# Optimization experiments

Hardware: AMD Instinct MI355X
Metric: run time of the kernel (lower is better)

Reference implementation:

```python
import jax, jax.numpy as jnp
import numpy as np

N_STEP = 64
GAMMA = 10.0
DIST_MIN, DIST_MAX = 0.0, 10.0
N_LAYER = 4
H_DIM, E_DIM, HID_DIM = 128, 16, 256
N_NODES, N_EDGES = 10000, 320000


def setup_inputs() -> dict:
    key = jax.random.key(0)
    ks = jax.random.split(key, 12)
    in_m = 2 * H_DIM + E_DIM + N_STEP  # 336
    s = 0.02
    return {
        "x": jax.random.normal(ks[0], (N_NODES, H_DIM), jnp.float32),
        "pos": jax.random.normal(ks[1], (N_NODES, 3), jnp.float32),
        "edge_index": jax.random.randint(ks[2], (2, N_EDGES), 0, N_NODES),
        "edge_attr": jax.random.normal(ks[3], (N_EDGES, E_DIM), jnp.float32),
        "Wm": jax.random.normal(ks[4], (N_LAYER, in_m, HID_DIM), jnp.float32) * s,
        "bm": jnp.zeros((N_LAYER, HID_DIM), jnp.float32),
        "Wp": jax.random.normal(ks[5], (N_LAYER, HID_DIM, 1), jnp.float32) * s,
        "bp": jnp.zeros((N_LAYER, 1), jnp.float32),
        "Wx": jax.random.normal(ks[6], (N_LAYER, H_DIM + HID_DIM, H_DIM), jnp.float32) * s,
        "bx": jnp.zeros((N_LAYER, H_DIM), jnp.float32),
    }


def _egnn_layer(x, pos, edge_index, edge_attr, Wm, bm, Wp, bp, Wx, bx):
    i, j = edge_index[0], edge_index[1]
    n = x.shape[0]
    x_i, x_j = x[i], x[j]                       # [E, h] gathers
    # NOTE: source uses x (not pos) for the distance feature -- replicated.
    r = jnp.linalg.norm(x_i - x_j, axis=1)      # [E]
    c = jnp.linspace(DIST_MIN, DIST_MAX, N_STEP, dtype=x.dtype)
    soh = jnp.exp(-GAMMA * (r[:, None] - c[None, :]) ** 2)  # [E, n_step]
    m_ij = jnp.concatenate([x_i, x_j, soh, edge_attr], axis=1) @ Wm + bm  # [E, hid]
    _alpha = m_ij @ Wp + bp  # computed but unused in source's _update_pos
    # position update: scatter-mean of pos_i - pos_j over destination i
    pos_vect = pos[i] - pos[j]                  # [E, 3]
    cnt = jax.ops.segment_sum(jnp.ones((i.shape[0],), pos.dtype), i, num_segments=n)
    pos_aggr = jax.ops.segment_sum(pos_vect, i, num_segments=n) / jnp.maximum(cnt, 1.0)[:, None]
    pos = pos + pos_aggr
    # feature update: scatter-sum of messages
    m_aggr = jax.ops.segment_sum(m_ij, i, num_segments=n)  # [N, hid]
    x = jnp.concatenate([x, m_aggr], axis=1) @ Wx + bx      # [N, h]
    return x, pos


def reference(x, pos, edge_index, edge_attr, Wm, bm, Wp, bp, Wx, bx):
    x_ori = x
    for l in range(N_LAYER):
        x, pos = _egnn_layer(x, pos, edge_index, edge_attr,
                             Wm[l], bm[l], Wp[l], bp[l], Wx[l], bx[l])
        x = jax.nn.leaky_relu(x)
    x = x_ori + x            # residual_connection == 'add'
    x = jax.nn.leaky_relu(x)  # activate_last
    return x, pos
```

## Files before the change

kernel.cpp:

```cpp
#include <hip/hip_runtime.h>
#include <hip/hip_bf16.h>

#define NN 10000
#define NE 320000
#define HD 128
#define ED 16
#define HID 256
#define KP 480
#define AST 488

typedef unsigned short ushort_t;
typedef __attribute__((ext_vector_type(8))) short short8;
typedef __attribute__((ext_vector_type(4))) float f32x4;

__device__ __forceinline__ float leaky(float v){ return v > 0.f ? v : 0.01f*v; }
__device__ __forceinline__ ushort_t f2bs(float v){
  __hip_bfloat16 b = __float2bfloat16(v);
  return *(ushort_t*)&b;
}
__device__ __forceinline__ unsigned pack2u(float a, float b){
  return (unsigned)f2bs(a) | ((unsigned)f2bs(b) << 16);
}
__device__ __forceinline__ float bl(unsigned u){ return __uint_as_float(u << 16); }
__device__ __forceinline__ float bh(unsigned u){ return __uint_as_float(u & 0xffff0000u); }
__device__ __forceinline__ float2 cvt2(unsigned u){ return make_float2(bl(u), bh(u)); }

__global__ __launch_bounds__(256) void k_misc(const float* __restrict__ x, ushort_t* __restrict__ xb,
                                              const int* __restrict__ ii, int* __restrict__ cnt,
                                              const float* __restrict__ Wx, ushort_t* __restrict__ WcT){
  int t = blockIdx.x*256 + threadIdx.x;
  if (t < NN*HD){
    xb[t] = f2bs(x[t]);
  } else if (t < NN*HD + NE){
    atomicAdd(&cnt[ii[t - NN*HD]], 1);
  } else if (t < NN*HD + NE + 4*HD*HD){
    int u = t - NN*HD - NE;
    int l = u >> 14, r = (u >> 7) & 127, c = u & 127;
    WcT[((long)l*HD + c)*KP + r] = f2bs(Wx[(long)l*(HD+HID)*HD + r*HD + c]);
  } else {
    int u = t - NN*HD - NE - 4*HD*HD;
    if (u < 4*HD*15){
      int row = u / 15, k = 465 + u % 15;
      WcT[(long)row*KP + k] = 0;
    }
  }
}

__global__ __launch_bounds__(256) void k_scan(const int* __restrict__ cnt, int* __restrict__ row_ptr){
  const int PER = 40;
  __shared__ int sh[256];
  int t = threadIdx.x;
  int base = t*PER;
  int s = 0;
  for (int k = 0; k < PER; ++k){ int idx = base+k; if (idx < NN) s += cnt[idx]; }
  sh[t] = s; __syncthreads();
  for (int off = 1; off < 256; off <<= 1){
    int v = (t >= off) ? sh[t-off] : 0;
    __syncthreads();
    sh[t] += v;
    __syncthreads();
  }
  int pre = sh[t] - s;
  for (int k = 0; k < PER; ++k){
    int idx = base+k;
    if (idx < NN){ row_ptr[idx] = pre; pre += cnt[idx]; }
  }
  if (t == 255) row_ptr[NN] = sh[255];
}

__global__ __launch_bounds__(256) void k_fillwc(const int* __restrict__ ii, const int* __restrict__ jj,
                                                const int* __restrict__ row_ptr, int* __restrict__ c2,
                                                int* __restrict__ sj, int* __restrict__ se,
                                                const float* __restrict__ Wm, const float* __restrict__ bm,
                                                const float* __restrict__ Wx, ushort_t* __restrict__ WcT){
  if (blockIdx.x < 1250){
    int e = blockIdx.x*256 + threadIdx.x;
    int a = ii[e];
    int p = atomicAdd(&c2[a], 1);
    int idx = row_ptr[a] + p;
    sj[idx] = jj[e];
    se[idx] = e;
    return;
  }
  __shared__ float a_s[16*36];
  __shared__ float w_s[16*128];
  int bi = blockIdx.x - 1250;
  int t  = threadIdx.x;
  int rb = (bi % 11) * 32;
  int l  = bi / 11;
  int lr = t >> 4, lk = t & 15;
  int wcc = t & 127, wk = t >> 7;
  int cg = t & 31, rg = t >> 5;
  const float* Wxb = Wx + (long)l*(HD+HID)*HD + HD*HD;
  float acc[4][4];
  #pragma unroll
  for (int i = 0; i < 4; ++i)
    #pragma unroll
    for (int j = 0; j < 4; ++j) acc[i][j] = 0.f;
  for (int k0 = 0; k0 < HID; k0 += 16){
    int m0 = rb + lr, m1 = rb + lr + 16;
    float v0 = 0.f, v1 = 0.f;
    if (m0 < 336) v0 = Wm[((long)l*336 + m0)*HID + k0 + lk];
    else if (m0 == 336) v0 = bm[l*HID + k0 + lk];
    if (m1 < 336) v1 = Wm[((long)l*336 + m1)*HID + k0 + lk];
    else if (m1 == 336) v1 = bm[l*HID + k0 + lk];
    a_s[lk*36 + lr]      = v0;
    a_s[lk*36 + lr + 16] = v1;
    #pragma unroll
    for (int q = 0; q < 8; ++q)
      w_s[(wk + 2*q)*128 + wcc] = Wxb[(k0 + wk + 2*q)*HD + wcc];
    __syncthreads();
    #pragma unroll
    for (int k = 0; k < 16; ++k){
      float4 av = *(const float4*)&a_s[k*36 + rg*4];
      float4 wv = *(const float4*)&w_s[k*128 + cg*4];
      acc[0][0] += av.x*wv.x; acc[0][1] += av.x*wv.y; acc[0][2] += av.x*wv.z; acc[0][3] += av.x*wv.w;
      acc[1][0] += av.y*wv.x; acc[1][1] += av.y*wv.y; acc[1][2] += av.y*wv.z; acc[1][3] += av.y*wv.w;
      acc[2][0] += av.z*wv.x; acc[2][1] += av.z*wv.y; acc[2][2] += av.z*wv.z; acc[2][3] += av.z*wv.w;
      acc[3][0] += av.w*wv.x; acc[3][1] += av.w*wv.y; acc[3][2] += av.w*wv.z; acc[3][3] += av.w*wv.w;
    }
    __syncthreads();
  }
  #pragma unroll
  for (int i = 0; i < 4; ++i){
    int m = rb + rg*4 + i;
    if (m < 337){
      #pragma unroll
      for (int j = 0; j < 4; ++j)
        WcT[((long)l*HD + cg*4 + j)*KP + 128 + m] = f2bs(acc[i][j]);
    }
  }
}

template<int FIRST, int FINAL>
__global__ __launch_bounds__(256) void k_layer(const uint4* __restrict__ xb4, const float* __restrict__ posf_cur,
                                               const int* __restrict__ row_ptr, const int* __restrict__ sj,
                                               const int* __restrict__ se, const float* __restrict__ ea,
                                               ushort_t* __restrict__ inv,
                                               const ushort_t* __restrict__ WcT, const float* __restrict__ bx,
                                               ushort_t* __restrict__ xb_next, const float* __restrict__ x_ori,
                                               float* __restrict__ out, float* __restrict__ posf_next){
  __shared__ ushort_t Asm[8*AST];
  int tid = threadIdx.x;
  int nl  = tid >> 5;
  int n   = blockIdx.x*8 + nl;
  int sub = tid & 31;
  int g   = sub >> 4;
  int gl  = sub & 15;
  int beg = row_ptr[n], end = row_ptr[n+1];
  int len = end - beg;
  int q0 = beg + ((len * g) >> 1);
  int q1 = beg + ((len * (g+1)) >> 1);

  uint4 xi = xb4[(long)n*16 + gl];
  float2 xi0 = cvt2(xi.x), xi1 = cvt2(xi.y), xi2 = cvt2(xi.z), xi3 = cvt2(xi.w);
  float c0 = (10.0f/63.0f)*(float)(4*gl);
  float c1 = (10.0f/63.0f)*(float)(4*gl+1);
  float c2 = (10.0f/63.0f)*(float)(4*gl+2);
  float c3 = (10.0f/63.0f)*(float)(4*gl+3);

  float2 s0 = {0,0}, s1 = {0,0}, s2 = {0,0}, s3 = {0,0};
  float h0 = 0, h1 = 0, h2 = 0, h3 = 0, sp = 0, sea = 0;

#define EPROC(Bv, Jv, Ev) { \
    float2 e0=cvt2(Bv.x), e1=cvt2(Bv.y), e2=cvt2(Bv.z), e3=cvt2(Bv.w); \
    float d, p=0.f; \
    d=xi0.x-e0.x; p+=d*d;  d=xi0.y-e0.y; p+=d*d; \
    d=xi1.x-e1.x; p+=d*d;  d=xi1.y-e1.y; p+=d*d; \
    d=xi2.x-e2.x; p+=d*d;  d=xi2.y-e2.y; p+=d*d; \
    d=xi3.x-e3.x; p+=d*d;  d=xi3.y-e3.y; p+=d*d; \
    p += __shfl_xor(p,1,64); p += __shfl_xor(p,2,64); \
    p += __shfl_xor(p,4,64); p += __shfl_xor(p,8,64); \
    float r = sqrtf(p); \
    float t0=r-c0, t1=r-c1, t2=r-c2, t3=r-c3; \
    h0 += __expf(-10.f*t0*t0); h1 += __expf(-10.f*t1*t1); \
    h2 += __expf(-10.f*t2*t2); h3 += __expf(-10.f*t3*t3); \
    s0.x+=e0.x; s0.y+=e0.y; s1.x+=e1.x; s1.y+=e1.y; \
    s2.x+=e2.x; s2.y+=e2.y; s3.x+=e3.x; s3.y+=e3.y; \
    if (FIRST) sea += ea[(long)(Ev)*ED + gl]; \
    if (gl < 3) sp += posf_cur[(long)Jv*3 + gl]; }

  int idx = q0;
  for (; idx + 3 < q1; idx += 4){
    int j0 = sj[idx], j1 = sj[idx+1], j2 = sj[idx+2], j3 = sj[idx+3];
    int e0i = FIRST ? se[idx]   : 0;
    int e1i = FIRST ? se[idx+1] : 0;
    int e2i = FIRST ? se[idx+2] : 0;
    int e3i = FIRST ? se[idx+3] : 0;
    uint4 B0 = xb4[(long)j0*16 + gl];
    uint4 B1 = xb4[(long)j1*16 + gl];
    uint4 B2 = xb4[(long)j2*16 + gl];
    uint4 B3 = xb4[(long)j3*16 + gl];
    EPROC(B0, j0, e0i); EPROC(B1, j1, e1i); EPROC(B2, j2, e2i); EPROC(B3, j3, e3i);
  }
  for (; idx < q1; ++idx){
    int j0 = sj[idx];
    int e0i = FIRST ? se[idx] : 0;
    uint4 B0 = xb4[(long)j0*16 + gl];
    EPROC(B0, j0, e0i);
  }
#undef EPROC

  s0.x += __shfl_xor(s0.x,16,64); s0.y += __shfl_xor(s0.y,16,64);
  s1.x += __shfl_xor(s1.x,16,64); s1.y += __shfl_xor(s1.y,16,64);
  s2.x += __shfl_xor(s2.x,16,64); s2.y += __shfl_xor(s2.y,16,64);
  s3.x += __shfl_xor(s3.x,16,64); s3.y += __shfl_xor(s3.y,16,64);
  h0 += __shfl_xor(h0,16,64); h1 += __shfl_xor(h1,16,64);
  h2 += __shfl_xor(h2,16,64); h3 += __shfl_xor(h3,16,64);
  sp += __shfl_xor(sp,16,64);
  if (FIRST) sea += __shfl_xor(sea,16,64);

  if (g == 0){
    float cf = (float)len;
    ushort_t* Ar = Asm + nl*AST;
    ((uint4*)Ar)[gl] = xi;
    ((uint4*)(Ar + 128))[gl] = make_uint4(pack2u(cf*xi0.x, cf*xi0.y), pack2u(cf*xi1.x, cf*xi1.y),
                                          pack2u(cf*xi2.x, cf*xi2.y), pack2u(cf*xi3.x, cf*xi3.y));
    ((uint4*)(Ar + 256))[gl] = make_uint4(pack2u(s0.x, s0.y), pack2u(s1.x, s1.y),
                                          pack2u(s2.x, s2.y), pack2u(s3.x, s3.y));
    ((uint2*)(Ar + 384))[gl] = make_uint2(pack2u(h0, h1), pack2u(h2, h3));
    ushort_t sea_us;
    if (FIRST){
      sea_us = f2bs(sea);
      inv[(long)n*16 + gl] = sea_us;
    } else {
      sea_us = inv[(long)n*16 + gl];
    }
    Ar[448 + gl] = sea_us;
    Ar[464 + gl] = (gl == 0) ? f2bs(cf) : (ushort_t)0;
    if (gl < 3){
      float pi = posf_cur[n*3 + gl];
      posf_next[n*3 + gl] = pi + (cf*pi - sp) / fmaxf(cf, 1.f);
    }
  }
  __syncthreads();

  int wave = tid >> 6, lane = tid & 63;
  int quad = lane >> 4, l16 = lane & 15;
  int nb = wave * 32;
  const ushort_t* Arow = Asm + (l16 & 7)*AST + quad*8;
  const ushort_t* W0 = WcT + (long)(nb + l16)*KP + quad*8;
  const ushort_t* W1 = WcT + (long)(nb + 16 + l16)*KP + quad*8;
  f32x4 acc0 = {0,0,0,0}, acc1 = {0,0,0,0};
  for (int k0 = 0; k0 < KP; k0 += 32){
    short8 av = *(const short8*)(Arow + k0);
    short8 b0 = *(const short8*)(W0 + k0);
    short8 b1 = *(const short8*)(W1 + k0);
    acc0 = __builtin_amdgcn_mfma_f32_16x16x32_bf16(av, b0, acc0, 0, 0, 0);
    acc1 = __builtin_amdgcn_mfma_f32_16x16x32_bf16(av, b1, acc1, 0, 0, 0);
  }
  float bx0 = bx[nb + l16], bx1 = bx[nb + 16 + l16];
  #pragma unroll
  for (int r = 0; r < 4; ++r){
    int row = quad*4 + r;
    if (row < 8){
      long base = (long)(blockIdx.x*8 + row)*HD;
      float v0 = leaky(acc0[r] + bx0);
      float v1 = leaky(acc1[r] + bx1);
      if (FINAL){
        out[base + nb + l16]      = leaky(x_ori[base + nb + l16] + v0);
        out[base + nb + 16 + l16] = leaky(x_ori[base + nb + 16 + l16] + v1);
      } else {
        xb_next[base + nb + l16]      = f2bs(v0);
        xb_next[base + nb + 16 + l16] = f2bs(v1);
      }
    }
  }
}

extern "C" void kernel_launch(void* const* d_in, const int* in_sizes, int n_in,
                              void* d_out, int out_size, void* d_ws, size_t ws_size,
                              hipStream_t stream){
  const float* x   = (const float*)d_in[0];
  const float* pos = (const float*)d_in[1];
  const int*   ei  = (const int*)d_in[2];
  const float* ea  = (const float*)d_in[3];
  const float* Wm  = (const float*)d_in[4];
  const float* bm  = (const float*)d_in[5];
  const float* Wx  = (const float*)d_in[8];
  const float* bx  = (const float*)d_in[9];
  float* out_x   = (float*)d_out;
  float* out_pos = out_x + NN*HD;

  ushort_t* xbA    = (ushort_t*)d_ws;
  ushort_t* xbB    = xbA + NN*HD;
  ushort_t* WcT    = xbB + NN*HD;
  ushort_t* inv    = WcT + 4*HD*KP;
  float*    pfA    = (float*)(inv + NN*16);
  float*    pfB    = pfA + NN*3;
  int*      cnt    = (int*)(pfB + NN*3);
  int*      c2     = cnt + NN;
  int*      row_ptr= c2 + NN;
  int*      sj     = row_ptr + (NN+1);
  int*      se     = sj + NE;
  const int* ii = ei;
  const int* jj = ei + NE;

  hipMemsetAsync(cnt, 0, 2*NN*sizeof(int), stream);
  int misc_threads = NN*HD + NE + 4*HD*HD + 4*HD*15;
  k_misc  <<<(misc_threads + 255)/256, 256, 0, stream>>>(x, xbA, ii, cnt, Wx, WcT);
  k_scan  <<<1, 256, 0, stream>>>(cnt, row_ptr);
  k_fillwc<<<1250 + 44, 256, 0, stream>>>(ii, jj, row_ptr, c2, sj, se, Wm, bm, Wx, WcT);

  const float* ps[4] = {pos, pfA, pfB, pfA};
  float*       pd[4] = {pfA, pfB, pfA, out_pos};

  k_layer<1,0><<<1250, 256, 0, stream>>>((const uint4*)xbA, ps[0], row_ptr, sj, se, ea, inv,
                                         WcT + 0*HD*KP, bx + 0*HD, xbB, x, out_x, pd[0]);
  k_layer<0,0><<<1250, 256, 0, stream>>>((const uint4*)xbB, ps[1], row_ptr, sj, se, ea, inv,
                                         WcT + 1*(long)HD*KP, bx + 1*HD, xbA, x, out_x, pd[1]);
  k_layer<0,0><<<1250, 256, 0, stream>>>((const uint4*)xbA, ps[2], row_ptr, sj, se, ea, inv,
                                         WcT + 2*(long)HD*KP, bx + 2*HD, xbB, x, out_x, pd[2]);
  k_layer<0,1><<<1250, 256, 0, stream>>>((const uint4*)xbB, ps[3], row_ptr, sj, se, ea, inv,
                                         WcT + 3*(long)HD*KP, bx + 3*HD, xbA, x, out_x, pd[3]);
}
```

Baseline: 334.7 us.

## Compress neighbor indices to 16-bit, use nontemporal loads, stage epilogue via LDS

Neighbor indices in the CSR arrays are stored as 16-bit values, which halves their memory traffic. This relies on node count fitting in 16 bits (10000 does). The index and edge-attribute streams are read with nontemporal loads so they do not pollute the cache. The layer epilogue now writes results to shared memory first and then emits coalesced 16-byte stores of the output rows, instead of scattered 2- and 4-byte stores. This adds an extra barrier and LDS usage per block.

```diff
diff --git a/kernel.cpp b/kernel.cpp
--- a/kernel.cpp
+++ b/kernel.cpp
@@ -24,6 +24,9 @@
 __device__ __forceinline__ float bl(unsigned u){ return __uint_as_float(u << 16); }
 __device__ __forceinline__ float bh(unsigned u){ return __uint_as_float(u & 0xffff0000u); }
 __device__ __forceinline__ float2 cvt2(unsigned u){ return make_float2(bl(u), bh(u)); }
+__device__ __forceinline__ int      ntl_i(const int* p){ return __builtin_nontemporal_load(p); }
+__device__ __forceinline__ ushort_t ntl_us(const ushort_t* p){ return __builtin_nontemporal_load(p); }
+__device__ __forceinline__ float    ntl_f(const float* p){ return __builtin_nontemporal_load(p); }
 
 __global__ __launch_bounds__(256) void k_misc(const float* __restrict__ x, ushort_t* __restrict__ xb,
                                               const int* __restrict__ ii, int* __restrict__ cnt,
@@ -70,7 +73,7 @@
 
 __global__ __launch_bounds__(256) void k_fillwc(const int* __restrict__ ii, const int* __restrict__ jj,
                                                 const int* __restrict__ row_ptr, int* __restrict__ c2,
-                                                int* __restrict__ sj, int* __restrict__ se,
+                                                ushort_t* __restrict__ sj, int* __restrict__ se,
                                                 const float* __restrict__ Wm, const float* __restrict__ bm,
                                                 const float* __restrict__ Wx, ushort_t* __restrict__ WcT){
   if (blockIdx.x < 1250){
@@ -78,7 +81,7 @@
     int a = ii[e];
     int p = atomicAdd(&c2[a], 1);
     int idx = row_ptr[a] + p;
-    sj[idx] = jj[e];
+    sj[idx] = (ushort_t)jj[e];
     se[idx] = e;
     return;
   }
@@ -134,13 +137,14 @@
 
 template<int FIRST, int FINAL>
 __global__ __launch_bounds__(256) void k_layer(const uint4* __restrict__ xb4, const float* __restrict__ posf_cur,
-                                               const int* __restrict__ row_ptr, const int* __restrict__ sj,
+                                               const int* __restrict__ row_ptr, const ushort_t* __restrict__ sj,
                                                const int* __restrict__ se, const float* __restrict__ ea,
                                                ushort_t* __restrict__ inv,
                                                const ushort_t* __restrict__ WcT, const float* __restrict__ bx,
                                                ushort_t* __restrict__ xb_next, const float* __restrict__ x_ori,
                                                float* __restrict__ out, float* __restrict__ posf_next){
   __shared__ ushort_t Asm[8*AST];
+  __shared__ float epi[8*128];
   int tid = threadIdx.x;
   int nl  = tid >> 5;
   int n   = blockIdx.x*8 + nl;
@@ -177,16 +181,18 @@
     h2 += __expf(-10.f*t2*t2); h3 += __expf(-10.f*t3*t3); \
     s0.x+=e0.x; s0.y+=e0.y; s1.x+=e1.x; s1.y+=e1.y; \
     s2.x+=e2.x; s2.y+=e2.y; s3.x+=e3.x; s3.y+=e3.y; \
-    if (FIRST) sea += ea[(long)(Ev)*ED + gl]; \
+    if (FIRST) sea += ntl_f(&ea[(long)(Ev)*ED + gl]); \
     if (gl < 3) sp += posf_cur[(long)Jv*3 + gl]; }
 
   int idx = q0;
   for (; idx + 3 < q1; idx += 4){
-    int j0 = sj[idx], j1 = sj[idx+1], j2 = sj[idx+2], j3 = sj[idx+3];
-    int e0i = FIRST ? se[idx]   : 0;
-    int e1i = FIRST ? se[idx+1] : 0;
-    int e2i = FIRST ? se[idx+2] : 0;
-    int e3i = FIRST ? se[idx+3] : 0;
+    int j0 = (int)ntl_us(&sj[idx]),   j1 = (int)ntl_us(&sj[idx+1]);
+    int j2 = (int)ntl_us(&sj[idx+2]), j3 = (int)ntl_us(&sj[idx+3]);
+    int e0i=0,e1i=0,e2i=0,e3i=0;
+    if (FIRST){
+      e0i = ntl_i(&se[idx]);   e1i = ntl_i(&se[idx+1]);
+      e2i = ntl_i(&se[idx+2]); e3i = ntl_i(&se[idx+3]);
+    }
     uint4 B0 = xb4[(long)j0*16 + gl];
     uint4 B1 = xb4[(long)j1*16 + gl];
     uint4 B2 = xb4[(long)j2*16 + gl];
@@ -194,8 +200,8 @@
     EPROC(B0, j0, e0i); EPROC(B1, j1, e1i); EPROC(B2, j2, e2i); EPROC(B3, j3, e3i);
   }
   for (; idx < q1; ++idx){
-    int j0 = sj[idx];
-    int e0i = FIRST ? se[idx] : 0;
+    int j0 = (int)ntl_us(&sj[idx]);
+    int e0i = FIRST ? ntl_i(&se[idx]) : 0;
     uint4 B0 = xb4[(long)j0*16 + gl];
     EPROC(B0, j0, e0i);
   }
@@ -250,20 +256,37 @@
     acc1 = __builtin_amdgcn_mfma_f32_16x16x32_bf16(av, b1, acc1, 0, 0, 0);
   }
   float bx0 = bx[nb + l16], bx1 = bx[nb + 16 + l16];
-  #pragma unroll
-  for (int r = 0; r < 4; ++r){
-    int row = quad*4 + r;
-    if (row < 8){
-      long base = (long)(blockIdx.x*8 + row)*HD;
+  if (quad < 2){
+    #pragma unroll
+    for (int r = 0; r < 4; ++r){
+      int row = quad*4 + r;
       float v0 = leaky(acc0[r] + bx0);
       float v1 = leaky(acc1[r] + bx1);
       if (FINAL){
-        out[base + nb + l16]      = leaky(x_ori[base + nb + l16] + v0);
-        out[base + nb + 16 + l16] = leaky(x_ori[base + nb + 16 + l16] + v1);
+        epi[row*128 + nb + l16]      = v0;
+        epi[row*128 + nb + 16 + l16] = v1;
       } else {
-        xb_next[base + nb + l16]      = f2bs(v0);
-        xb_next[base + nb + 16 + l16] = f2bs(v1);
+        ushort_t* eu = (ushort_t*)epi;
+        eu[row*128 + nb + l16]      = f2bs(v0);
+        eu[row*128 + nb + 16 + l16] = f2bs(v1);
       }
+    }
+  }
+  __syncthreads();
+  if (FINAL){
+    int row = tid >> 5, seg = tid & 31;
+    long gbase = ((long)(blockIdx.x*8 + row)*HD) + seg*4;
+    float4 v = ((const float4*)epi)[row*32 + seg];
+    float4 xo = *(const float4*)(x_ori + gbase);
+    float4 o;
+    o.x = leaky(xo.x + v.x); o.y = leaky(xo.y + v.y);
+    o.z = leaky(xo.z + v.z); o.w = leaky(xo.w + v.w);
+    *(float4*)(out + gbase) = o;
+  } else {
+    if (tid < 128){
+      int row = tid >> 4, seg = tid & 15;
+      uint4 v = ((const uint4*)epi)[row*16 + seg];
+      ((uint4*)xb_next)[(long)(blockIdx.x*8 + row)*16 + seg] = v;
     }
   }
 }
@@ -286,13 +309,13 @@
   ushort_t* xbB    = xbA + NN*HD;
   ushort_t* WcT    = xbB + NN*HD;
   ushort_t* inv    = WcT + 4*HD*KP;
-  float*    pfA    = (float*)(inv + NN*16);
+  ushort_t* sj     = inv + NN*16;
+  float*    pfA    = (float*)(sj + NE);
   float*    pfB    = pfA + NN*3;
   int*      cnt    = (int*)(pfB + NN*3);
   int*      c2     = cnt + NN;
   int*      row_ptr= c2 + NN;
-  int*      sj     = row_ptr + (NN+1);
-  int*      se     = sj + NE;
+  int*      se     = row_ptr + (NN+1);
   const int* ii = ei;
   const int* jj = ei + NE;
 
```

After: 354.4 us. 1.06x slower.
